# Kernel optimization log

Measured on AMD Instinct MI355X. Metric: run time of the kernel, lower is better.

## Reference

```python
import jax, jax.numpy as jnp
import numpy as np

NNZ = 16777216  # 2**24 nonzeros
D = 2048        # dense size (D, D, D); sum over dim 2 -> (D, D)


def setup_inputs() -> dict:
    key = jax.random.key(0)
    kv, ki = jax.random.split(key)
    values = jax.random.normal(kv, (NNZ,), dtype=jnp.float32)
    indices = jax.random.randint(ki, (3, NNZ), 0, D, dtype=jnp.int64)
    return {"values": values, "indices": indices}


def reference(values, indices):
    # sparse_coo_tensor(indices, values, size=(D,D,D)) -> sparse.sum(dim=2) -> to_dense()
    # is equivalent to a scatter-add of values keyed by (indices[0], indices[1]):
    # the third index only distinguishes entries that get summed away, and COO
    # coalescing already sums duplicate coordinates.
    out = jnp.zeros((D, D), dtype=jnp.float32)
    out = out.at[indices[0], indices[1]].add(values)
    return out
```

## Files before the change

kernel.cpp:

```cpp
#include <hip/hip_runtime.h>

#define NNZ 16777216
#define D 2048
#define NB 256
#define ROWS_PER_B 8
#define T1 512
#define EPT 16
#define CHUNK 8192
#define NCHUNK (NNZ / CHUNK)
#define SEG 8960
#define T2 512
#define NW (T2 / 64)
#define RUNS (NCHUNK / NW)
#define DEPTH 8

__global__ __launch_bounds__(T1) void bin_scatter(
    const float* __restrict__ values,
    const int* __restrict__ idx0,
    const int* __restrict__ idx1,
    unsigned int* __restrict__ dump,
    unsigned int* __restrict__ pptabT)
{
    __shared__ unsigned int lhist[NB];
    __shared__ unsigned int ppref[NB];
    __shared__ unsigned int wsum[4];
    __shared__ unsigned int stage[SEG];

    const int tid = threadIdx.x;
    if (tid < NB) lhist[tid] = 0;
    __syncthreads();

    const int vecBase = blockIdx.x * (CHUNK / 4);

    float4 v[4]; int4 a[4]; int4 c[4];
#pragma unroll
    for (int it = 0; it < 4; ++it) {
        int g = vecBase + it * T1 + tid;
        v[it] = reinterpret_cast<const float4*>(values)[g];
        a[it] = reinterpret_cast<const int4*>(idx0)[g];
        c[it] = reinterpret_cast<const int4*>(idx1)[g];
    }

    unsigned int outw[EPT];
    unsigned int meta[EPT];
#pragma unroll
    for (int it = 0; it < 4; ++it) {
        const int*   ap = reinterpret_cast<const int*>(&a[it]);
        const int*   cp = reinterpret_cast<const int*>(&c[it]);
        const float* vp = reinterpret_cast<const float*>(&v[it]);
#pragma unroll
        for (int e = 0; e < 4; ++e) {
            int i0 = ap[e], i1 = cp[e];
            unsigned int b = (unsigned int)i0 >> 3;
            unsigned int fb = __float_as_uint(vp[e]);
            unsigned int bf = (fb + 0x7fffu + ((fb >> 16) & 1u)) >> 16;
            outw[it * 4 + e] = ((((unsigned int)(i0 & 7) << 11) | (unsigned int)i1) << 16) | bf;
            unsigned int rk = atomicAdd(&lhist[b], 1u);
            meta[it * 4 + e] = (b << 16) | rk;
        }
    }
    __syncthreads();

    unsigned int x = 0, pc = 0, cnt = 0;
    if (tid < NB) {
        const int lane = tid & 63;
        cnt = lhist[tid];
        pc = (cnt + 3u) & ~3u;
        x = pc;
#pragma unroll
        for (int dlt = 1; dlt < 64; dlt <<= 1) {
            unsigned int y = __shfl_up(x, dlt, 64);
            if (lane >= dlt) x += y;
        }
        if (lane == 63) wsum[tid >> 6] = x;
    }
    __syncthreads();
    if (tid < NB) {
        const int wid = tid >> 6;
        unsigned int off = 0;
#pragma unroll
        for (int w = 0; w < 4; ++w) off += (w < wid) ? wsum[w] : 0u;
        unsigned int excl = x - pc + off;
        ppref[tid] = excl;
        pptabT[(size_t)tid * NCHUNK + blockIdx.x] = (excl << 16) | cnt;
    }
    __syncthreads();

#pragma unroll
    for (int e = 0; e < EPT; ++e) {
        unsigned int b  = meta[e] >> 16;
        unsigned int rk = meta[e] & 0xFFFFu;
        stage[ppref[b] + rk] = outw[e];
    }
    __syncthreads();

    const uint4* s4 = reinterpret_cast<const uint4*>(stage);
    uint4* d4 = reinterpret_cast<uint4*>(dump + (size_t)blockIdx.x * SEG);
    for (int j = tid; j < SEG / 4; j += T1)
        d4[j] = s4[j];
}

__global__ __launch_bounds__(T2) void bucket_accumulate(
    const unsigned int* __restrict__ dump,
    const unsigned int* __restrict__ pptabT,
    float* __restrict__ out)
{
    __shared__ float tile[ROWS_PER_B * D];
    __shared__ unsigned int sdesc[NCHUNK];

    const int b = blockIdx.x;
    const int tid = threadIdx.x;
    const int w = tid >> 6;
    const int lane = tid & 63;

    for (int j = tid; j < ROWS_PER_B * D / 4; j += T2)
        reinterpret_cast<float4*>(tile)[j] = make_float4(0.f, 0.f, 0.f, 0.f);
    for (int j = tid; j < NCHUNK; j += T2)
        sdesc[j] = pptabT[(size_t)b * NCHUNK + j];
    __syncthreads();

    const unsigned int k0 = (unsigned int)w * RUNS;

    unsigned int pc0, pc1, pc2, pc3, pc4, pc5, pc6, pc7;
    unsigned int wd0, wd1, wd2, wd3, wd4, wd5, wd6, wd7;

#define PAYLOAD(kn, pcv) \
    ((lane < (int)((pcv) & 0xFFFFu)) \
        ? dump[(kn) * SEG + ((pcv) >> 16) + (unsigned)lane] : 0u)

    pc0 = sdesc[k0 + 0]; pc1 = sdesc[k0 + 1]; pc2 = sdesc[k0 + 2]; pc3 = sdesc[k0 + 3];
    pc4 = sdesc[k0 + 4]; pc5 = sdesc[k0 + 5]; pc6 = sdesc[k0 + 6]; pc7 = sdesc[k0 + 7];
    wd0 = PAYLOAD(k0 + 0, pc0); wd1 = PAYLOAD(k0 + 1, pc1);
    wd2 = PAYLOAD(k0 + 2, pc2); wd3 = PAYLOAD(k0 + 3, pc3);
    wd4 = PAYLOAD(k0 + 4, pc4); wd5 = PAYLOAD(k0 + 5, pc5);
    wd6 = PAYLOAD(k0 + 6, pc6); wd7 = PAYLOAD(k0 + 7, pc7);

#define PSTEP(i, pcv, wdv) { \
    if (wdv) atomicAdd(&tile[wdv >> 16], __uint_as_float(wdv << 16)); \
    unsigned int c_ = pcv & 0xFFFFu; \
    if (c_ > 64u) {                        \
        const unsigned int* base_ = dump + (k0 + (unsigned)(j + i)) * SEG + (pcv >> 16); \
        for (unsigned int t_ = 64u + (unsigned)lane; t_ < c_; t_ += 64u) { \
            unsigned int ww_ = base_[t_]; \
            if (ww_) atomicAdd(&tile[ww_ >> 16], __uint_as_float(ww_ << 16)); \
        } \
    } \
    int jn_ = j + i + DEPTH; \
    if (jn_ < RUNS) { \
        unsigned int pcn_ = sdesc[k0 + (unsigned)jn_];    \
        wdv = PAYLOAD(k0 + (unsigned)jn_, pcn_); \
        pcv = pcn_; \
    } else { wdv = 0u; pcv = 0u; } \
}

    for (int j = 0; j < RUNS; j += DEPTH) {
        PSTEP(0, pc0, wd0) PSTEP(1, pc1, wd1) PSTEP(2, pc2, wd2) PSTEP(3, pc3, wd3)
        PSTEP(4, pc4, wd4) PSTEP(5, pc5, wd5) PSTEP(6, pc6, wd6) PSTEP(7, pc7, wd7)
    }
#undef PSTEP
#undef PAYLOAD
    __syncthreads();

    float4* o4 = reinterpret_cast<float4*>(out + (size_t)b * ROWS_PER_B * D);
    for (int j = tid; j < ROWS_PER_B * D / 4; j += T2)
        o4[j] = reinterpret_cast<float4*>(tile)[j];
}

__global__ __launch_bounds__(256) void scatter_add_kernel(
    const float* __restrict__ values,
    const int* __restrict__ idx0,
    const int* __restrict__ idx1,
    float* __restrict__ out)
{
    const int nvec = NNZ / 4;
    int tid = blockIdx.x * blockDim.x + threadIdx.x;
    int stride = gridDim.x * blockDim.x;
    for (int i = tid; i < nvec; i += stride) {
        const float4 v = reinterpret_cast<const float4*>(values)[i];
        const int4   a = reinterpret_cast<const int4*>(idx0)[i];
        const int4   b = reinterpret_cast<const int4*>(idx1)[i];
        atomicAdd(&out[a.x * D + b.x], v.x);
        atomicAdd(&out[a.y * D + b.y], v.y);
        atomicAdd(&out[a.z * D + b.z], v.z);
        atomicAdd(&out[a.w * D + b.w], v.w);
    }
}

extern "C" void kernel_launch(void* const* d_in, const int* in_sizes, int n_in,
                              void* d_out, int out_size, void* d_ws, size_t ws_size,
                              hipStream_t stream) {
    const float* values  = (const float*)d_in[0];
    const int*   indices = (const int*)d_in[1];
    const int*   idx0 = indices;
    const int*   idx1 = indices + NNZ;
    float* out = (float*)d_out;

    const size_t pp_bytes = (size_t)NB * NCHUNK * sizeof(unsigned int);
    const size_t need = pp_bytes + (size_t)NCHUNK * SEG * sizeof(unsigned int);

    if (ws_size < need) {
        hipMemsetAsync(out, 0, (size_t)out_size * sizeof(float), stream);
        const int nvec = NNZ / 4;
        scatter_add_kernel<<<(nvec + 255) / 256, 256, 0, stream>>>(values, idx0, idx1, out);
        return;
    }

    unsigned int* pptabT = (unsigned int*)d_ws;
    unsigned int* dump   = (unsigned int*)((char*)d_ws + pp_bytes);

    bin_scatter<<<NCHUNK, T1, 0, stream>>>(values, idx0, idx1, dump, pptabT);
    bucket_accumulate<<<NB, T2, 0, stream>>>(dump, pptabT, out);
}
```

Measured before the change: 150.8 us.

## Hoist overflow runs out of pipelined loop and double block size in accumulate

Doubles the accumulate kernel's block to 1024 threads, so each wave handles fewer chunk runs. The rare overflow entries (runs longer than 64) move out of the per-wave pipeline into a separate pass where each thread walks one chunk's overflow serially. The main loop becomes branch-free and loads descriptors with vectorized uint4 shared-memory reads. The aim is to remove divergent inner loops from the latency-bound prefetch pipeline and raise memory-level parallelism, at the cost of more LDS atomic contention per block and a serial per-thread overflow walk.

Measured after the change: 146.8 us. 2.7% less time.

```diff
diff --git a/kernel.cpp b/kernel.cpp
--- a/kernel.cpp
+++ b/kernel.cpp
@@ -9,10 +9,9 @@
 #define CHUNK 8192
 #define NCHUNK (NNZ / CHUNK)
 #define SEG 8960
-#define T2 512
+#define T2 1024
 #define NW (T2 / 64)
 #define RUNS (NCHUNK / NW)
-#define DEPTH 8
 
 __global__ __launch_bounds__(T1) void bin_scatter(
     const float* __restrict__ values,
@@ -119,45 +118,54 @@
         sdesc[j] = pptabT[(size_t)b * NCHUNK + j];
     __syncthreads();
 
+    for (int j = tid; j < NCHUNK; j += T2) {
+        unsigned int d = sdesc[j];
+        unsigned int c = d & 0xFFFFu;
+        if (c > 64u) {
+            const unsigned int* base = dump + (unsigned int)j * SEG + (d >> 16);
+            for (unsigned int t = 64u; t < c; ++t) {
+                unsigned int ww = base[t];
+                if (ww) atomicAdd(&tile[ww >> 16], __uint_as_float(ww << 16));
+            }
+        }
+    }
+
     const unsigned int k0 = (unsigned int)w * RUNS;
 
-    unsigned int pc0, pc1, pc2, pc3, pc4, pc5, pc6, pc7;
+#define PAYLOAD(kn, dsc) \
+    ((lane < (int)((dsc) & 0xFFFFu)) \
+        ? dump[(unsigned int)(kn) * SEG + ((dsc) >> 16) + (unsigned int)lane] : 0u)
+#define ACC(wdv) if (wdv) atomicAdd(&tile[(wdv) >> 16], __uint_as_float((wdv) << 16));
+
     unsigned int wd0, wd1, wd2, wd3, wd4, wd5, wd6, wd7;
-
-#define PAYLOAD(kn, pcv) \
-    ((lane < (int)((pcv) & 0xFFFFu)) \
-        ? dump[(kn) * SEG + ((pcv) >> 16) + (unsigned)lane] : 0u)
-
-    pc0 = sdesc[k0 + 0]; pc1 = sdesc[k0 + 1]; pc2 = sdesc[k0 + 2]; pc3 = sdesc[k0 + 3];
-    pc4 = sdesc[k0 + 4]; pc5 = sdesc[k0 + 5]; pc6 = sdesc[k0 + 6]; pc7 = sdesc[k0 + 7];
-    wd0 = PAYLOAD(k0 + 0, pc0); wd1 = PAYLOAD(k0 + 1, pc1);
-    wd2 = PAYLOAD(k0 + 2, pc2); wd3 = PAYLOAD(k0 + 3, pc3);
-    wd4 = PAYLOAD(k0 + 4, pc4); wd5 = PAYLOAD(k0 + 5, pc5);
-    wd6 = PAYLOAD(k0 + 6, pc6); wd7 = PAYLOAD(k0 + 7, pc7);
-
-#define PSTEP(i, pcv, wdv) { \
-    if (wdv) atomicAdd(&tile[wdv >> 16], __uint_as_float(wdv << 16)); \
-    unsigned int c_ = pcv & 0xFFFFu; \
-    if (c_ > 64u) {                        \
-        const unsigned int* base_ = dump + (k0 + (unsigned)(j + i)) * SEG + (pcv >> 16); \
-        for (unsigned int t_ = 64u + (unsigned)lane; t_ < c_; t_ += 64u) { \
-            unsigned int ww_ = base_[t_]; \
-            if (ww_) atomicAdd(&tile[ww_ >> 16], __uint_as_float(ww_ << 16)); \
-        } \
-    } \
-    int jn_ = j + i + DEPTH; \
-    if (jn_ < RUNS) { \
-        unsigned int pcn_ = sdesc[k0 + (unsigned)jn_];    \
-        wdv = PAYLOAD(k0 + (unsigned)jn_, pcn_); \
-        pcv = pcn_; \
-    } else { wdv = 0u; pcv = 0u; } \
-}
-
-    for (int j = 0; j < RUNS; j += DEPTH) {
-        PSTEP(0, pc0, wd0) PSTEP(1, pc1, wd1) PSTEP(2, pc2, wd2) PSTEP(3, pc3, wd3)
-        PSTEP(4, pc4, wd4) PSTEP(5, pc5, wd5) PSTEP(6, pc6, wd6) PSTEP(7, pc7, wd7)
-    }
-#undef PSTEP
+    {
+        uint4 qa = *reinterpret_cast<const uint4*>(&sdesc[k0]);
+        uint4 qb = *reinterpret_cast<const uint4*>(&sdesc[k0 + 4]);
+        wd0 = PAYLOAD(k0 + 0, qa.x); wd1 = PAYLOAD(k0 + 1, qa.y);
+        wd2 = PAYLOAD(k0 + 2, qa.z); wd3 = PAYLOAD(k0 + 3, qa.w);
+        wd4 = PAYLOAD(k0 + 4, qb.x); wd5 = PAYLOAD(k0 + 5, qb.y);
+        wd6 = PAYLOAD(k0 + 6, qb.z); wd7 = PAYLOAD(k0 + 7, qb.w);
+    }
+
+    for (int j = 0; j < RUNS; j += 8) {
+        unsigned int nd0 = 0, nd1 = 0, nd2 = 0, nd3 = 0,
+                     nd4 = 0, nd5 = 0, nd6 = 0, nd7 = 0;
+        if (j + 8 < RUNS) {
+            uint4 na = *reinterpret_cast<const uint4*>(&sdesc[k0 + j + 8]);
+            uint4 nb = *reinterpret_cast<const uint4*>(&sdesc[k0 + j + 12]);
+            nd0 = na.x; nd1 = na.y; nd2 = na.z; nd3 = na.w;
+            nd4 = nb.x; nd5 = nb.y; nd6 = nb.z; nd7 = nb.w;
+        }
+        ACC(wd0) wd0 = PAYLOAD(k0 + j + 8,  nd0);
+        ACC(wd1) wd1 = PAYLOAD(k0 + j + 9,  nd1);
+        ACC(wd2) wd2 = PAYLOAD(k0 + j + 10, nd2);
+        ACC(wd3) wd3 = PAYLOAD(k0 + j + 11, nd3);
+        ACC(wd4) wd4 = PAYLOAD(k0 + j + 12, nd4);
+        ACC(wd5) wd5 = PAYLOAD(k0 + j + 13, nd5);
+        ACC(wd6) wd6 = PAYLOAD(k0 + j + 14, nd6);
+        ACC(wd7) wd7 = PAYLOAD(k0 + j + 15, nd7);
+    }
+#undef ACC
 #undef PAYLOAD
     __syncthreads();
 
```
